# Optimization experiments

Hardware: AMD Instinct MI355X
Metric: run time of the kernel (lower is better)

## Reference

```python
import jax, jax.numpy as jnp
import numpy as np

NUM_EXPERTS = 8
TOP_K = 2


def setup_inputs() -> dict:
    key = jax.random.key(0)
    ks = jax.random.split(key, 6)
    B, S, D, F, E = 2, 2048, 512, 1536, NUM_EXPERTS
    scale = 0.02
    return {
        "x": jax.random.normal(ks[0], (B, S, D), dtype=jnp.float32),
        "Wg": jax.random.normal(ks[1], (D, E), dtype=jnp.float32) * scale,
        "W1": jax.random.normal(ks[2], (E, D, F), dtype=jnp.float32) * scale,
        "W2": jax.random.normal(ks[3], (E, F, D), dtype=jnp.float32) * scale,
        "W3": jax.random.normal(ks[4], (E, D, F), dtype=jnp.float32) * scale,
        "b3": jax.random.normal(ks[5], (E, F), dtype=jnp.float32) * scale,
    }


def reference(x, Wg, W1, W2, W3, b3):
    # Router (eval mode: no noise). x: [B,S,D]
    logits = jnp.einsum("bsd,de->bse", x, Wg)  # [B,S,E]
    top_logits, top_idx = jax.lax.top_k(logits, TOP_K)  # [B,S,K]
    top_w = jax.nn.softmax(top_logits, axis=-1)  # [B,S,K]
    # Combine weights per expert: scatter top-k weights into E slots.
    onehot = jax.nn.one_hot(top_idx, NUM_EXPERTS, dtype=x.dtype)  # [B,S,K,E]
    C = jnp.sum(onehot * top_w[..., None], axis=-2)  # [B,S,E]
    # Dense per-expert SwiGLU FFN; non-selected experts contribute weight 0,
    # so the math matches the original masked gather/scatter exactly.
    h = jnp.einsum("bsd,edf->bsef", x, W1)  # [B,S,E,F]
    g = jnp.einsum("bsd,edf->bsef", x, W3) + b3  # [B,S,E,F]
    act = jax.nn.silu(h) * g  # [B,S,E,F]
    out = jnp.einsum("bse,bsef,efd->bsd", C, act, W2)  # [B,S,D]
    return out
```

## Files before the change

### kernel.cpp

```cpp
#include <hip/hip_runtime.h>

constexpr int NTOK = 4096;
constexpr int DIM  = 512;
constexpr int FF   = 1536;
constexpr int NE   = 8;
constexpr int CAP  = 4096;

typedef __attribute__((ext_vector_type(8))) short short8;
typedef __attribute__((ext_vector_type(4))) float f32x4;

static __device__ __forceinline__ unsigned short f2bf(float f) {
    unsigned int x = __float_as_uint(f);
    unsigned int r = x + 0x7fffu + ((x >> 16) & 1u);
    return (unsigned short)(r >> 16);
}

static __device__ __forceinline__ void gload_lds16(const void* g, void* l) {
    __builtin_amdgcn_global_load_lds(
        (const __attribute__((address_space(1))) unsigned int*)g,
        (__attribute__((address_space(3))) unsigned int*)l, 16, 0, 0);
}

__global__ __launch_bounds__(256) void moe_router(
    const float* __restrict__ x, const float* __restrict__ wg,
    int* __restrict__ eidx, float* __restrict__ wts)
{
    int lane = threadIdx.x & 63;
    int wave = threadIdx.x >> 6;
    int tok  = blockIdx.x * 4 + wave;

    float acc[NE];
#pragma unroll
    for (int e = 0; e < NE; ++e) acc[e] = 0.f;

    const float* xr = x + (size_t)tok * DIM;
#pragma unroll
    for (int i = 0; i < DIM / 64; ++i) {
        int d = i * 64 + lane;
        float xv = xr[d];
        const float4* wr = (const float4*)(wg + (size_t)d * NE);
        float4 w0 = wr[0], w1 = wr[1];
        acc[0] += xv * w0.x; acc[1] += xv * w0.y; acc[2] += xv * w0.z; acc[3] += xv * w0.w;
        acc[4] += xv * w1.x; acc[5] += xv * w1.y; acc[6] += xv * w1.z; acc[7] += xv * w1.w;
    }
#pragma unroll
    for (int e = 0; e < NE; ++e) {
#pragma unroll
        for (int off = 32; off >= 1; off >>= 1)
            acc[e] += __shfl_xor(acc[e], off, 64);
    }
    if (lane == 0) {
        int i0 = 0; float m0 = acc[0];
#pragma unroll
        for (int e = 1; e < NE; ++e) if (acc[e] > m0) { m0 = acc[e]; i0 = e; }
        int i1 = -1; float m1 = -3.4e38f;
#pragma unroll
        for (int e = 0; e < NE; ++e) if (e != i0 && acc[e] > m1) { m1 = acc[e]; i1 = e; }
        float e1 = expf(m1 - m0);
        float s  = 1.f + e1;
        int s0 = tok * 2, s1 = tok * 2 + 1;
        wts[s0] = 1.f / s;
        wts[s1] = e1 / s;
        eidx[s0] = i0;
        eidx[s1] = i1;
    }
}

__global__ __launch_bounds__(256) void moe_build_lists(
    const int* __restrict__ eidx, int* __restrict__ cnt, int* __restrict__ lists)
{
    int e = blockIdx.x;
    __shared__ int s_base;
    __shared__ int s_wcnt[4];
    if (threadIdx.x == 0) s_base = 0;
    __syncthreads();
    int lane = threadIdx.x & 63, wv = threadIdx.x >> 6;
    for (int c = 0; c < 2 * NTOK; c += 256) {
        int slot = c + threadIdx.x;
        bool m = (eidx[slot] == e);
        unsigned long long bal = __ballot(m);
        if (lane == 0) s_wcnt[wv] = __popcll(bal);
        __syncthreads();
        int wbase = s_base;
        for (int i = 0; i < wv; ++i) wbase += s_wcnt[i];
        if (m) {
            int off = __popcll(bal & ((1ull << lane) - 1ull));
            lists[e * CAP + wbase + off] = slot;
        }
        __syncthreads();
        if (threadIdx.x == 0) s_base += s_wcnt[0] + s_wcnt[1] + s_wcnt[2] + s_wcnt[3];
        __syncthreads();
    }
    if (threadIdx.x == 0) cnt[e] = s_base;
}

__global__ __launch_bounds__(256) void cvt_x(
    const float* __restrict__ x, unsigned short* __restrict__ xbf)
{
    int i = (blockIdx.x * 256 + threadIdx.x) * 8;
    float4 a = *(const float4*)(x + i);
    float4 b = *(const float4*)(x + i + 4);
    ushort4 o0, o1;
    o0.x = f2bf(a.x); o0.y = f2bf(a.y); o0.z = f2bf(a.z); o0.w = f2bf(a.w);
    o1.x = f2bf(b.x); o1.y = f2bf(b.y); o1.z = f2bf(b.z); o1.w = f2bf(b.w);
    *(ushort4*)(xbf + i)     = o0;
    *(ushort4*)(xbf + i + 4) = o1;
}

__global__ __launch_bounds__(256) void transpose_cvt(
    const float* __restrict__ in, unsigned short* __restrict__ out, int R, int C)
{
    __shared__ float tile[64][65];
    int c0 = blockIdx.x * 64;
    int r0 = blockIdx.y * 64;
    int z  = blockIdx.z;
    const float* ip = in + (size_t)z * R * C;
    char* op = (char*)(out + (size_t)z * R * C);

    int tr = threadIdx.x >> 4;
    int tc = (threadIdx.x & 15) * 4;
#pragma unroll
    for (int p = 0; p < 4; ++p) {
        int r = p * 16 + tr;
        float4 v = *(const float4*)(ip + (size_t)(r0 + r) * C + c0 + tc);
        tile[r][tc + 0] = v.x; tile[r][tc + 1] = v.y;
        tile[r][tc + 2] = v.z; tile[r][tc + 3] = v.w;
    }
    __syncthreads();
#pragma unroll
    for (int p = 0; p < 4; ++p) {
        int c = p * 16 + tr;
        ushort4 o;
        o.x = f2bf(tile[tc + 0][c]);
        o.y = f2bf(tile[tc + 1][c]);
        o.z = f2bf(tile[tc + 2][c]);
        o.w = f2bf(tile[tc + 3][c]);
        int cb = ((r0 + tc) * 2) ^ ((c & 7) << 4);
        *(ushort4*)(op + (size_t)(c0 + c) * (R * 2) + cb) = o;
    }
}

__global__ __launch_bounds__(256) void moe_ffn1(
    const unsigned short* __restrict__ xbf,
    const unsigned short* __restrict__ w1t,
    const unsigned short* __restrict__ w3t,
    const float* __restrict__ b3,
    const int* __restrict__ cnt, const int* __restrict__ lists,
    unsigned short* __restrict__ act)
{
    int e    = blockIdx.y >> 5;
    int mb   = blockIdx.y & 31;
    int n0   = blockIdx.x * 64;
    int ce   = cnt[e];
    int row0 = mb * 128;
    if (row0 >= ce) return;

    __shared__ int s_slot[128];
    __shared__ __attribute__((aligned(16))) char sA [128 * 128];
    __shared__ __attribute__((aligned(16))) char sB1[64 * 128];
    __shared__ __attribute__((aligned(16))) char sB3[64 * 128];

    int tid = threadIdx.x;
    if (tid < 128) {
        int r = row0 + tid;
        s_slot[tid] = (r < ce) ? lists[e * CAP + r] : lists[e * CAP + row0];
    }
    __syncthreads();

    int lane = tid & 63;
    int wv   = tid >> 6;
    int wm   = wv >> 1, wn = wv & 1;

    int lrow = lane >> 3;
    int lcol = (lane & 7) * 16;
    int aswz = lcol ^ (lrow << 4);
    const char* aSrc[4];
#pragma unroll
    for (int i = 0; i < 4; ++i) {
        int rr  = i * 32 + wv * 8 + lrow;
        int tok = s_slot[rr] >> 1;
        aSrc[i] = (const char*)xbf + (size_t)tok * (DIM * 2) + aswz;
    }
    const char* b1Src[2]; const char* b3Src[2];
#pragma unroll
    for (int i = 0; i < 2; ++i) {
        int rr = i * 32 + wv * 8 + lrow;
        size_t rb = ((size_t)e * FF + n0 + rr) * (DIM * 2) + lcol;
        b1Src[i] = (const char*)w1t + rb;
        b3Src[i] = (const char*)w3t + rb;
    }

    f32x4 acch[4][2], accg[4][2];
#pragma unroll
    for (int i = 0; i < 4; ++i)
#pragma unroll
        for (int j = 0; j < 2; ++j) { acch[i][j] = (f32x4)0.f; accg[i][j] = (f32x4)0.f; }

    for (int kc = 0; kc < DIM * 2; kc += 128) {
#pragma unroll
        for (int i = 0; i < 4; ++i)
            gload_lds16(aSrc[i] + kc, sA + (i * 32 + wv * 8) * 128);
#pragma unroll
        for (int i = 0; i < 2; ++i) {
            gload_lds16(b1Src[i] + kc, sB1 + (i * 32 + wv * 8) * 128);
            gload_lds16(b3Src[i] + kc, sB3 + (i * 32 + wv * 8) * 128);
        }
        __syncthreads();

#pragma unroll
        for (int ks = 0; ks < 2; ++ks) {
            short8 af[4], b1f[2], b3f[2];
#pragma unroll
            for (int mi = 0; mi < 4; ++mi) {
                int row = wm * 64 + mi * 16 + (lane & 15);
                int ba  = row * 128 + ((ks * 64 + (lane >> 4) * 16) ^ ((row & 7) << 4));
                af[mi] = *(const short8*)(sA + ba);
            }
#pragma unroll
            for (int ni = 0; ni < 2; ++ni) {
                int row = wn * 32 + ni * 16 + (lane & 15);
                int ba  = row * 128 + ((ks * 64 + (lane >> 4) * 16) ^ ((row & 7) << 4));
                b1f[ni] = *(const short8*)(sB1 + ba);
                b3f[ni] = *(const short8*)(sB3 + ba);
            }
#pragma unroll
            for (int mi = 0; mi < 4; ++mi)
#pragma unroll
                for (int ni = 0; ni < 2; ++ni) {
                    acch[mi][ni] = __builtin_amdgcn_mfma_f32_16x16x32_bf16(af[mi], b1f[ni], acch[mi][ni], 0, 0, 0);
                    accg[mi][ni] = __builtin_amdgcn_mfma_f32_16x16x32_bf16(af[mi], b3f[ni], accg[mi][ni], 0, 0, 0);
                }
        }
        __syncthreads();
    }

#pragma unroll
    for (int ni = 0; ni < 2; ++ni) {
        int fcol = n0 + wn * 32 + ni * 16 + (lane & 15);
        float b3v = b3[e * FF + fcol];
#pragma unroll
        for (int mi = 0; mi < 4; ++mi) {
            int rl = wm * 64 + mi * 16 + (lane >> 4) * 4;
#pragma unroll
            for (int r = 0; r < 4; ++r) {
                int rg = rl + r;
                if (row0 + rg < ce) {
                    float h = acch[mi][ni][r];
                    float g = accg[mi][ni][r] + b3v;
                    float a = (h / (1.f + __expf(-h))) * g;
                    act[(size_t)s_slot[rg] * FF + fcol] = f2bf(a);
                }
            }
        }
    }
}

__global__ __launch_bounds__(256) void moe_ffn2(
    const unsigned short* __restrict__ act,
    const unsigned short* __restrict__ w2t,
    const int* __restrict__ cnt, const int* __restrict__ lists,
    const float* __restrict__ wts,
    float* __restrict__ yws)
{
    int e    = blockIdx.y >> 5;
    int mb   = blockIdx.y & 31;
    int n0   = blockIdx.x * 64;
    int ce   = cnt[e];
    int row0 = mb * 128;
    if (row0 >= ce) return;

    __shared__ int   s_slot[128];
    __shared__ float s_w[128];
    __shared__ __attribute__((aligned(16))) char sA[128 * 128];
    __shared__ __attribute__((aligned(16))) char sB[64 * 128];

    int tid = threadIdx.x;
    if (tid < 128) {
        int r  = row0 + tid;
        int sl = (r < ce) ? lists[e * CAP + r] : lists[e * CAP + row0];
        s_slot[tid] = sl;
        s_w[tid]    = wts[sl];
    }
    __syncthreads();

    int lane = tid & 63;
    int wv   = tid >> 6;
    int wm   = wv >> 1, wn = wv & 1;

    int lrow = lane >> 3;
    int lcol = (lane & 7) * 16;
    int aswz = lcol ^ (lrow << 4);
    const char* aSrc[4];
#pragma unroll
    for (int i = 0; i < 4; ++i) {
        int rr = i * 32 + wv * 8 + lrow;
        aSrc[i] = (const char*)act + (size_t)s_slot[rr] * (FF * 2) + aswz;
    }
    const char* bSrc[2];
#pragma unroll
    for (int i = 0; i < 2; ++i) {
        int rr = i * 32 + wv * 8 + lrow;
        bSrc[i] = (const char*)w2t + ((size_t)e * DIM + n0 + rr) * (FF * 2) + lcol;
    }

    f32x4 acc[4][2];
#pragma unroll
    for (int i = 0; i < 4; ++i)
#pragma unroll
        for (int j = 0; j < 2; ++j) acc[i][j] = (f32x4)0.f;

    for (int kc = 0; kc < FF * 2; kc += 128) {
#pragma unroll
        for (int i = 0; i < 4; ++i)
            gload_lds16(aSrc[i] + kc, sA + (i * 32 + wv * 8) * 128);
#pragma unroll
        for (int i = 0; i < 2; ++i)
            gload_lds16(bSrc[i] + kc, sB + (i * 32 + wv * 8) * 128);
        __syncthreads();

#pragma unroll
        for (int ks = 0; ks < 2; ++ks) {
            short8 af[4], bf[2];
#pragma unroll
            for (int mi = 0; mi < 4; ++mi) {
                int row = wm * 64 + mi * 16 + (lane & 15);
                int ba  = row * 128 + ((ks * 64 + (lane >> 4) * 16) ^ ((row & 7) << 4));
                af[mi] = *(const short8*)(sA + ba);
            }
#pragma unroll
            for (int ni = 0; ni < 2; ++ni) {
                int row = wn * 32 + ni * 16 + (lane & 15);
                int ba  = row * 128 + ((ks * 64 + (lane >> 4) * 16) ^ ((row & 7) << 4));
                bf[ni] = *(const short8*)(sB + ba);
            }
#pragma unroll
            for (int mi = 0; mi < 4; ++mi)
#pragma unroll
                for (int ni = 0; ni < 2; ++ni)
                    acc[mi][ni] = __builtin_amdgcn_mfma_f32_16x16x32_bf16(af[mi], bf[ni], acc[mi][ni], 0, 0, 0);
        }
        __syncthreads();
    }

#pragma unroll
    for (int mi = 0; mi < 4; ++mi) {
#pragma unroll
        for (int r = 0; r < 4; ++r) {
            int rg = wm * 64 + mi * 16 + (lane >> 4) * 4 + r;
            if (row0 + rg < ce) {
                float w  = s_w[rg];
                int slot = s_slot[rg];
#pragma unroll
                for (int ni = 0; ni < 2; ++ni) {
                    int dd = n0 + wn * 32 + ni * 16 + (lane & 15);
                    yws[(size_t)slot * DIM + dd] = acc[mi][ni][r] * w;
                }
            }
        }
    }
}

__global__ __launch_bounds__(256) void moe_combine(
    const float* __restrict__ yws, float* __restrict__ out)
{
    int i  = blockIdx.x * 256 + threadIdx.x;
    int t  = i >> 7;
    int d4 = (i & 127) * 4;
    const float4* y0 = (const float4*)(yws + ((size_t)(2 * t)     * DIM + d4));
    const float4* y1 = (const float4*)(yws + ((size_t)(2 * t + 1) * DIM + d4));
    float4 a = *y0, b = *y1;
    float4 o = make_float4(a.x + b.x, a.y + b.y, a.z + b.z, a.w + b.w);
    *(float4*)(out + (size_t)t * DIM + d4) = o;
}

extern "C" void kernel_launch(void* const* d_in, const int* in_sizes, int n_in,
                              void* d_out, int out_size, void* d_ws, size_t ws_size,
                              hipStream_t stream)
{
    const float* x  = (const float*)d_in[0];
    const float* wg = (const float*)d_in[1];
    const float* w1 = (const float*)d_in[2];
    const float* w2 = (const float*)d_in[3];
    const float* w3 = (const float*)d_in[4];
    const float* b3 = (const float*)d_in[5];
    float* out = (float*)d_out;
    char*  ws  = (char*)d_ws;

    int*   cnt   = (int*)ws;
    int*   lists = (int*)(ws + 256);
    float* wts   = (float*)(ws + 256 + NE * CAP * 4);
    int*   eidx  = (int*)(ws + 256 + NE * CAP * 4 + NTOK * 2 * 4);
    size_t off   = 256 + (size_t)NE * CAP * 4 + (size_t)NTOK * 2 * 4 * 2;

    constexpr size_t WSZ = (size_t)NE * DIM * FF;
    unsigned short* w2t = (unsigned short*)(ws + off);
    unsigned short* w1t = w2t + WSZ;
    unsigned short* w3t = w1t + WSZ;
    unsigned short* act = w3t + WSZ;
    unsigned short* xbf = w2t;
    float*          yws = (float*)w1t;

    moe_router<<<NTOK / 4, 256, 0, stream>>>(x, wg, eidx, wts);
    moe_build_lists<<<NE, 256, 0, stream>>>(eidx, cnt, lists);
    cvt_x<<<NTOK * DIM / 8 / 256, 256, 0, stream>>>(x, xbf);

    dim3 tgA(FF / 64, DIM / 64, NE);
    transpose_cvt<<<tgA, 256, 0, stream>>>(w1, w1t, DIM, FF);
    transpose_cvt<<<tgA, 256, 0, stream>>>(w3, w3t, DIM, FF);

    dim3 g1(FF / 64, NE * 32);
    moe_ffn1<<<g1, 256, 0, stream>>>(xbf, w1t, w3t, b3, cnt, lists, act);

    dim3 tgB(DIM / 64, FF / 64, NE);
    transpose_cvt<<<tgB, 256, 0, stream>>>(w2, w2t, FF, DIM);

    dim3 g2(DIM / 64, NE * 32);
    moe_ffn2<<<g2, 256, 0, stream>>>(act, w2t, cnt, lists, wts, yws);

    moe_combine<<<(NTOK * DIM / 4) / 256, 256, 0, stream>>>(yws, out);
}
```

Baseline: 266.0 us.

## Parallelize routing lists, fuse conversions, compact activations, widen FFN1 tiles

Several changes land together. The bf16 conversion of x moves into the router kernel, and the serial per-expert list build is replaced by a parallel count-then-scatter into one compact list. The W1/W3 transposes are merged into a single launch. FFN1 now uses 128-wide N tiles and writes activations contiguously per expert through an LDS-staged, swizzled coalesced store, so FFN2 reads contiguous rows instead of gathering by slot. FFN2 also stages its output through LDS for float4 scattered stores. The cost is larger register and LDS use in FFN1, which may lower occupancy.

```diff
diff --git a/kernel.cpp b/kernel.cpp
--- a/kernel.cpp
+++ b/kernel.cpp
@@ -4,7 +4,6 @@
 constexpr int DIM  = 512;
 constexpr int FF   = 1536;
 constexpr int NE   = 8;
-constexpr int CAP  = 4096;
 
 typedef __attribute__((ext_vector_type(8))) short short8;
 typedef __attribute__((ext_vector_type(4))) float f32x4;
@@ -23,7 +22,7 @@
 
 __global__ __launch_bounds__(256) void moe_router(
     const float* __restrict__ x, const float* __restrict__ wg,
-    int* __restrict__ eidx, float* __restrict__ wts)
+    int* __restrict__ eidx, float* __restrict__ wts, unsigned short* __restrict__ xbf)
 {
     int lane = threadIdx.x & 63;
     int wave = threadIdx.x >> 6;
@@ -34,10 +33,12 @@
     for (int e = 0; e < NE; ++e) acc[e] = 0.f;
 
     const float* xr = x + (size_t)tok * DIM;
+    unsigned short* xo = xbf + (size_t)tok * DIM;
 #pragma unroll
     for (int i = 0; i < DIM / 64; ++i) {
         int d = i * 64 + lane;
         float xv = xr[d];
+        xo[d] = f2bf(xv);
         const float4* wr = (const float4*)(wg + (size_t)d * NE);
         float4 w0 = wr[0], w1 = wr[1];
         acc[0] += xv * w0.x; acc[1] += xv * w0.y; acc[2] += xv * w0.z; acc[3] += xv * w0.w;
@@ -66,56 +67,77 @@
     }
 }
 
-__global__ __launch_bounds__(256) void moe_build_lists(
-    const int* __restrict__ eidx, int* __restrict__ cnt, int* __restrict__ lists)
-{
-    int e = blockIdx.x;
-    __shared__ int s_base;
-    __shared__ int s_wcnt[4];
-    if (threadIdx.x == 0) s_base = 0;
-    __syncthreads();
-    int lane = threadIdx.x & 63, wv = threadIdx.x >> 6;
-    for (int c = 0; c < 2 * NTOK; c += 256) {
-        int slot = c + threadIdx.x;
-        bool m = (eidx[slot] == e);
-        unsigned long long bal = __ballot(m);
-        if (lane == 0) s_wcnt[wv] = __popcll(bal);
-        __syncthreads();
-        int wbase = s_base;
-        for (int i = 0; i < wv; ++i) wbase += s_wcnt[i];
-        if (m) {
-            int off = __popcll(bal & ((1ull << lane) - 1ull));
-            lists[e * CAP + wbase + off] = slot;
-        }
-        __syncthreads();
-        if (threadIdx.x == 0) s_base += s_wcnt[0] + s_wcnt[1] + s_wcnt[2] + s_wcnt[3];
-        __syncthreads();
-    }
-    if (threadIdx.x == 0) cnt[e] = s_base;
-}
-
-__global__ __launch_bounds__(256) void cvt_x(
-    const float* __restrict__ x, unsigned short* __restrict__ xbf)
-{
-    int i = (blockIdx.x * 256 + threadIdx.x) * 8;
-    float4 a = *(const float4*)(x + i);
-    float4 b = *(const float4*)(x + i + 4);
-    ushort4 o0, o1;
-    o0.x = f2bf(a.x); o0.y = f2bf(a.y); o0.z = f2bf(a.z); o0.w = f2bf(a.w);
-    o1.x = f2bf(b.x); o1.y = f2bf(b.y); o1.z = f2bf(b.z); o1.w = f2bf(b.w);
-    *(ushort4*)(xbf + i)     = o0;
-    *(ushort4*)(xbf + i + 4) = o1;
-}
-
-__global__ __launch_bounds__(256) void transpose_cvt(
-    const float* __restrict__ in, unsigned short* __restrict__ out, int R, int C)
+__global__ __launch_bounds__(256) void moe_count(
+    const int* __restrict__ eidx, int* __restrict__ pcnt)
+{
+    __shared__ int s_wc[4][8];
+    int tid = threadIdx.x, lane = tid & 63, wv = tid >> 6;
+    int e = eidx[blockIdx.x * 256 + tid];
+#pragma unroll
+    for (int e0 = 0; e0 < 8; ++e0) {
+        unsigned long long bal = __ballot(e == e0);
+        if (lane == 0) s_wc[wv][e0] = __popcll(bal);
+    }
+    __syncthreads();
+    if (tid < 8)
+        pcnt[blockIdx.x * 8 + tid] = s_wc[0][tid] + s_wc[1][tid] + s_wc[2][tid] + s_wc[3][tid];
+}
+
+__global__ __launch_bounds__(256) void moe_scatter(
+    const int* __restrict__ eidx, const int* __restrict__ pcnt,
+    int* __restrict__ clist, int* __restrict__ cnt, int* __restrict__ ebase)
+{
+    __shared__ int s_all[256];
+    __shared__ int s_wc[4][8];
+    int tid = threadIdx.x, bx = blockIdx.x;
+    int lane = tid & 63, wv = tid >> 6;
+    s_all[tid] = pcnt[tid];
+    int slot = bx * 256 + tid;
+    int e = eidx[slot];
+    int myoff = 0;
+#pragma unroll
+    for (int e0 = 0; e0 < 8; ++e0) {
+        unsigned long long bal = __ballot(e == e0);
+        if (lane == 0) s_wc[wv][e0] = __popcll(bal);
+        if (e == e0) myoff = __popcll(bal & ((1ull << lane) - 1ull));
+    }
+    __syncthreads();
+    int base = 0;
+#pragma unroll
+    for (int ep = 0; ep < 8; ++ep) {
+        int t = 0;
+        for (int b = 0; b < 32; ++b) t += s_all[b * 8 + ep];
+        if (ep < e) base += (t + 7) & ~7;
+    }
+    int cbase = 0;
+    for (int b = 0; b < bx; ++b) cbase += s_all[b * 8 + e];
+    int wbase = 0;
+    for (int w = 0; w < wv; ++w) wbase += s_wc[w][e];
+    clist[base + cbase + wbase + myoff] = slot;
+    if (bx == 0 && tid == 0) {
+        int eb = 0;
+        for (int ep = 0; ep < 8; ++ep) {
+            int t = 0;
+            for (int b = 0; b < 32; ++b) t += s_all[b * 8 + ep];
+            cnt[ep] = t;
+            ebase[ep] = eb;
+            eb += (t + 7) & ~7;
+        }
+    }
+}
+
+__global__ __launch_bounds__(256) void transpose_cvt2(
+    const float* __restrict__ inA, unsigned short* __restrict__ outA,
+    const float* __restrict__ inB, unsigned short* __restrict__ outB,
+    int R, int C)
 {
     __shared__ float tile[64][65];
-    int c0 = blockIdx.x * 64;
-    int r0 = blockIdx.y * 64;
-    int z  = blockIdx.z;
-    const float* ip = in + (size_t)z * R * C;
-    char* op = (char*)(out + (size_t)z * R * C);
+    int c0 = blockIdx.x * 64, r0 = blockIdx.y * 64, z = blockIdx.z;
+    const float* in      = (z < 8) ? inA  : inB;
+    unsigned short* out  = (z < 8) ? outA : outB;
+    int zz = z & 7;
+    const float* ip = in + (size_t)zz * R * C;
+    char* op = (char*)(out + (size_t)zz * R * C);
 
     int tr = threadIdx.x >> 4;
     int tc = (threadIdx.x & 15) * 4;
@@ -140,13 +162,133 @@
     }
 }
 
-__global__ __launch_bounds__(256) void moe_ffn1(
+__global__ __launch_bounds__(256, 2) void moe_ffn1(
     const unsigned short* __restrict__ xbf,
     const unsigned short* __restrict__ w1t,
     const unsigned short* __restrict__ w3t,
     const float* __restrict__ b3,
-    const int* __restrict__ cnt, const int* __restrict__ lists,
-    unsigned short* __restrict__ act)
+    const int* __restrict__ cnt, const int* __restrict__ ebase,
+    const int* __restrict__ clist,
+    unsigned short* __restrict__ actc)
+{
+    int e    = blockIdx.y >> 5;
+    int mb   = blockIdx.y & 31;
+    int n0   = blockIdx.x * 128;
+    int ce   = cnt[e];
+    int row0 = mb * 128;
+    if (row0 >= ce) return;
+    int eb   = ebase[e];
+
+    __shared__ __attribute__((aligned(16))) char smem[49152];
+    __shared__ int s_slot[128];
+    char* sA  = smem;
+    char* sB1 = smem + 16384;
+    char* sB3 = smem + 32768;
+
+    int tid = threadIdx.x;
+    if (tid < 128) {
+        int r = row0 + tid;
+        s_slot[tid] = (r < ce) ? clist[eb + r] : clist[eb + row0];
+    }
+    __syncthreads();
+
+    int lane = tid & 63, wv = tid >> 6;
+    int wm = wv >> 1, wn = wv & 1;
+    int lrow = lane >> 3;
+    int lcol = (lane & 7) * 16;
+    int aswz = lcol ^ (lrow << 4);
+
+    const char* aSrc[4]; const char* b1Src[4]; const char* b3Src[4];
+#pragma unroll
+    for (int i = 0; i < 4; ++i) {
+        int rr = i * 32 + wv * 8 + lrow;
+        aSrc[i] = (const char*)xbf + (size_t)(s_slot[rr] >> 1) * (DIM * 2) + aswz;
+        size_t rb = ((size_t)e * FF + n0 + rr) * (DIM * 2) + lcol;
+        b1Src[i] = (const char*)w1t + rb;
+        b3Src[i] = (const char*)w3t + rb;
+    }
+
+    f32x4 acch[4][4], accg[4][4];
+#pragma unroll
+    for (int i = 0; i < 4; ++i)
+#pragma unroll
+        for (int j = 0; j < 4; ++j) { acch[i][j] = (f32x4)0.f; accg[i][j] = (f32x4)0.f; }
+
+    for (int kc = 0; kc < DIM * 2; kc += 128) {
+#pragma unroll
+        for (int i = 0; i < 4; ++i) {
+            int ro = (i * 32 + wv * 8) * 128;
+            gload_lds16(aSrc[i]  + kc, sA  + ro);
+            gload_lds16(b1Src[i] + kc, sB1 + ro);
+            gload_lds16(b3Src[i] + kc, sB3 + ro);
+        }
+        __syncthreads();
+
+#pragma unroll
+        for (int ks = 0; ks < 2; ++ks) {
+            short8 af[4], b1f[4], b3f[4];
+#pragma unroll
+            for (int mi = 0; mi < 4; ++mi) {
+                int row = wm * 64 + mi * 16 + (lane & 15);
+                int ba  = row * 128 + ((ks * 64 + (lane >> 4) * 16) ^ ((row & 7) << 4));
+                af[mi] = *(const short8*)(sA + ba);
+            }
+#pragma unroll
+            for (int ni = 0; ni < 4; ++ni) {
+                int row = wn * 64 + ni * 16 + (lane & 15);
+                int ba  = row * 128 + ((ks * 64 + (lane >> 4) * 16) ^ ((row & 7) << 4));
+                b1f[ni] = *(const short8*)(sB1 + ba);
+                b3f[ni] = *(const short8*)(sB3 + ba);
+            }
+#pragma unroll
+            for (int mi = 0; mi < 4; ++mi)
+#pragma unroll
+                for (int ni = 0; ni < 4; ++ni) {
+                    acch[mi][ni] = __builtin_amdgcn_mfma_f32_16x16x32_bf16(af[mi], b1f[ni], acch[mi][ni], 0, 0, 0);
+                    accg[mi][ni] = __builtin_amdgcn_mfma_f32_16x16x32_bf16(af[mi], b3f[ni], accg[mi][ni], 0, 0, 0);
+                }
+        }
+        __syncthreads();
+    }
+
+    char* sE = smem;
+#pragma unroll
+    for (int ni = 0; ni < 4; ++ni) {
+        int col = wn * 64 + ni * 16 + (lane & 15);
+        float b3v = b3[e * FF + n0 + col];
+#pragma unroll
+        for (int mi = 0; mi < 4; ++mi) {
+            int rbase = wm * 64 + mi * 16 + (lane >> 4) * 4;
+#pragma unroll
+            for (int r = 0; r < 4; ++r) {
+                float h = acch[mi][ni][r];
+                float g = accg[mi][ni][r] + b3v;
+                float a = (h / (1.f + __expf(-h))) * g;
+                *(unsigned short*)(sE + (rbase + r) * 256 + col * 2) = f2bf(a);
+            }
+        }
+    }
+    __syncthreads();
+
+    int lim = ce - row0;
+#pragma unroll
+    for (int it = 0; it < 8; ++it) {
+        int chunk = it * 256 + tid;
+        int row = chunk >> 4, c8 = chunk & 15;
+        if (row < lim) {
+            int crow = eb + row0 + row;
+            size_t dst = (size_t)crow * (FF * 2) + n0 * 2 + ((c8 * 16) ^ ((crow & 7) << 4));
+            *(short8*)((char*)actc + dst) = *(const short8*)(sE + row * 256 + c8 * 16);
+        }
+    }
+}
+
+__global__ __launch_bounds__(256) void moe_ffn2(
+    const unsigned short* __restrict__ actc,
+    const unsigned short* __restrict__ w2t,
+    const int* __restrict__ cnt, const int* __restrict__ ebase,
+    const int* __restrict__ clist, const float* __restrict__ wts,
+    float* __restrict__ yws)
 {
     int e    = blockIdx.y >> 5;
     int mb   = blockIdx.y & 31;
@@ -154,62 +296,60 @@
     int ce   = cnt[e];
     int row0 = mb * 128;
     if (row0 >= ce) return;
-
-    __shared__ int s_slot[128];
-    __shared__ __attribute__((aligned(16))) char sA [128 * 128];
-    __shared__ __attribute__((aligned(16))) char sB1[64 * 128];
-    __shared__ __attribute__((aligned(16))) char sB3[64 * 128];
+    int eb   = ebase[e];
+
+    __shared__ __attribute__((aligned(16))) char smem[32768];
+    __shared__ int   s_slot[128];
+    __shared__ float s_w[128];
+    char* sA = smem;
+    char* sB = smem + 16384;
 
     int tid = threadIdx.x;
     if (tid < 128) {
-        int r = row0 + tid;
-        s_slot[tid] = (r < ce) ? lists[e * CAP + r] : lists[e * CAP + row0];
-    }
-    __syncthreads();
-
-    int lane = tid & 63;
-    int wv   = tid >> 6;
-    int wm   = wv >> 1, wn = wv & 1;
-
+        int r  = row0 + tid;
+        int sl = (r < ce) ? clist[eb + r] : clist[eb + row0];
+        s_slot[tid] = sl;
+        s_w[tid]    = wts[sl];
+    }
+    __syncthreads();
+
+    int lane = tid & 63, wv = tid >> 6;
+    int wm = wv >> 1, wn = wv & 1;
     int lrow = lane >> 3;
     int lcol = (lane & 7) * 16;
-    int aswz = lcol ^ (lrow << 4);
+
     const char* aSrc[4];
 #pragma unroll
     for (int i = 0; i < 4; ++i) {
-        int rr  = i * 32 + wv * 8 + lrow;
-        int tok = s_slot[rr] >> 1;
-        aSrc[i] = (const char*)xbf + (size_t)tok * (DIM * 2) + aswz;
-    }
-    const char* b1Src[2]; const char* b3Src[2];
+        int rr = i * 32 + wv * 8 + lrow;
+        int cr = (row0 + rr < ce) ? (eb + row0 + rr) : (eb + row0);
+        aSrc[i] = (const char*)actc + (size_t)cr * (FF * 2) + lcol;
+    }
+    const char* bSrc[2];
 #pragma unroll
     for (int i = 0; i < 2; ++i) {
         int rr = i * 32 + wv * 8 + lrow;
-        size_t rb = ((size_t)e * FF + n0 + rr) * (DIM * 2) + lcol;
-        b1Src[i] = (const char*)w1t + rb;
-        b3Src[i] = (const char*)w3t + rb;
-    }
-
-    f32x4 acch[4][2], accg[4][2];
+        bSrc[i] = (const char*)w2t + ((size_t)e * DIM + n0 + rr) * (FF * 2) + lcol;
+    }
+
+    f32x4 acc[4][2];
 #pragma unroll
     for (int i = 0; i < 4; ++i)
 #pragma unroll
-        for (int j = 0; j < 2; ++j) { acch[i][j] = (f32x4)0.f; accg[i][j] = (f32x4)0.f; }
-
-    for (int kc = 0; kc < DIM * 2; kc += 128) {
+        for (int j = 0; j < 2; ++j) acc[i][j] = (f32x4)0.f;
+
+    for (int kc = 0; kc < FF * 2; kc += 128) {
 #pragma unroll
         for (int i = 0; i < 4; ++i)
             gload_lds16(aSrc[i] + kc, sA + (i * 32 + wv * 8) * 128);
 #pragma unroll
-        for (int i = 0; i < 2; ++i) {
-            gload_lds16(b1Src[i] + kc, sB1 + (i * 32 + wv * 8) * 128);
-            gload_lds16(b3Src[i] + kc, sB3 + (i * 32 + wv * 8) * 128);
-        }
+        for (int i = 0; i < 2; ++i)
+            gload_lds16(bSrc[i] + kc, sB + (i * 32 + wv * 8) * 128);
         __syncthreads();
 
 #pragma unroll
         for (int ks = 0; ks < 2; ++ks) {
-            short8 af[4], b1f[2], b3f[2];
+            short8 af[4], bf[2];
 #pragma unroll
             for (int mi = 0; mi < 4; ++mi) {
                 int row = wm * 64 + mi * 16 + (lane & 15);
@@ -220,117 +360,6 @@
             for (int ni = 0; ni < 2; ++ni) {
                 int row = wn * 32 + ni * 16 + (lane & 15);
                 int ba  = row * 128 + ((ks * 64 + (lane >> 4) * 16) ^ ((row & 7) << 4));
-                b1f[ni] = *(const short8*)(sB1 + ba);
-                b3f[ni] = *(const short8*)(sB3 + ba);
-            }
-#pragma unroll
-            for (int mi = 0; mi < 4; ++mi)
-#pragma unroll
-                for (int ni = 0; ni < 2; ++ni) {
-                    acch[mi][ni] = __builtin_amdgcn_mfma_f32_16x16x32_bf16(af[mi], b1f[ni], acch[mi][ni], 0, 0, 0);
-                    accg[mi][ni] = __builtin_amdgcn_mfma_f32_16x16x32_bf16(af[mi], b3f[ni], accg[mi][ni], 0, 0, 0);
-                }
-        }
-        __syncthreads();
-    }
-
-#pragma unroll
-    for (int ni = 0; ni < 2; ++ni) {
-        int fcol = n0 + wn * 32 + ni * 16 + (lane & 15);
-        float b3v = b3[e * FF + fcol];
-#pragma unroll
-        for (int mi = 0; mi < 4; ++mi) {
-            int rl = wm * 64 + mi * 16 + (lane >> 4) * 4;
-#pragma unroll
-            for (int r = 0; r < 4; ++r) {
-                int rg = rl + r;
-                if (row0 + rg < ce) {
-                    float h = acch[mi][ni][r];
-                    float g = accg[mi][ni][r] + b3v;
-                    float a = (h / (1.f + __expf(-h))) * g;
-                    act[(size_t)s_slot[rg] * FF + fcol] = f2bf(a);
-                }
-            }
-        }
-    }
-}
-
-__global__ __launch_bounds__(256) void moe_ffn2(
-    const unsigned short* __restrict__ act,
-    const unsigned short* __restrict__ w2t,
-    const int* __restrict__ cnt, const int* __restrict__ lists,
-    const float* __restrict__ wts,
-    float* __restrict__ yws)
-{
-    int e    = blockIdx.y >> 5;
-    int mb   = blockIdx.y & 31;
-    int n0   = blockIdx.x * 64;
-    int ce   = cnt[e];
-    int row0 = mb * 128;
-    if (row0 >= ce) return;
-
-    __shared__ int   s_slot[128];
-    __shared__ float s_w[128];
-    __shared__ __attribute__((aligned(16))) char sA[128 * 128];
-    __shared__ __attribute__((aligned(16))) char sB[64 * 128];
-
-    int tid = threadIdx.x;
-    if (tid < 128) {
-        int r  = row0 + tid;
-        int sl = (r < ce) ? lists[e * CAP + r] : lists[e * CAP + row0];
-        s_slot[tid] = sl;
-        s_w[tid]    = wts[sl];
-    }
-    __syncthreads();
-
-    int lane = tid & 63;
-    int wv   = tid >> 6;
-    int wm   = wv >> 1, wn = wv & 1;
-
-    int lrow = lane >> 3;
-    int lcol = (lane & 7) * 16;
-    int aswz = lcol ^ (lrow << 4);
-    const char* aSrc[4];
-#pragma unroll
-    for (int i = 0; i < 4; ++i) {
-        int rr = i * 32 + wv * 8 + lrow;
-        aSrc[i] = (const char*)act + (size_t)s_slot[rr] * (FF * 2) + aswz;
-    }
-    const char* bSrc[2];
-#pragma unroll
-    for (int i = 0; i < 2; ++i) {
-        int rr = i * 32 + wv * 8 + lrow;
-        bSrc[i] = (const char*)w2t + ((size_t)e * DIM + n0 + rr) * (FF * 2) + lcol;
-    }
-
-    f32x4 acc[4][2];
-#pragma unroll
-    for (int i = 0; i < 4; ++i)
-#pragma unroll
-        for (int j = 0; j < 2; ++j) acc[i][j] = (f32x4)0.f;
-
-    for (int kc = 0; kc < FF * 2; kc += 128) {
-#pragma unroll
-        for (int i = 0; i < 4; ++i)
-            gload_lds16(aSrc[i] + kc, sA + (i * 32 + wv * 8) * 128);
-#pragma unroll
-        for (int i = 0; i < 2; ++i)
-            gload_lds16(bSrc[i] + kc, sB + (i * 32 + wv * 8) * 128);
-        __syncthreads();
-
-#pragma unroll
-        for (int ks = 0; ks < 2; ++ks) {
-            short8 af[4], bf[2];
-#pragma unroll
-            for (int mi = 0; mi < 4; ++mi) {
-                int row = wm * 64 + mi * 16 + (lane & 15);
-                int ba  = row * 128 + ((ks * 64 + (lane >> 4) * 16) ^ ((row & 7) << 4));
-                af[mi] = *(const short8*)(sA + ba);
-            }
-#pragma unroll
-            for (int ni = 0; ni < 2; ++ni) {
-                int row = wn * 32 + ni * 16 + (lane & 15);
-                int ba  = row * 128 + ((ks * 64 + (lane >> 4) * 16) ^ ((row & 7) << 4));
                 bf[ni] = *(const short8*)(sB + ba);
             }
 #pragma unroll
@@ -342,21 +371,31 @@
         __syncthreads();
     }
 
+    char* sE = smem;
 #pragma unroll
     for (int mi = 0; mi < 4; ++mi) {
+        int rbase = wm * 64 + mi * 16 + (lane >> 4) * 4;
 #pragma unroll
         for (int r = 0; r < 4; ++r) {
-            int rg = wm * 64 + mi * 16 + (lane >> 4) * 4 + r;
-            if (row0 + rg < ce) {
-                float w  = s_w[rg];
-                int slot = s_slot[rg];
-#pragma unroll
-                for (int ni = 0; ni < 2; ++ni) {
-                    int dd = n0 + wn * 32 + ni * 16 + (lane & 15);
-                    yws[(size_t)slot * DIM + dd] = acc[mi][ni][r] * w;
-                }
-            }
-        }
+            int row = rbase + r;
+            float w = s_w[row];
+#pragma unroll
+            for (int ni = 0; ni < 2; ++ni) {
+                int col = wn * 32 + ni * 16 + (lane & 15);
+                *(float*)(sE + row * 256 + col * 4) = acc[mi][ni][r] * w;
+            }
+        }
+    }
+    __syncthreads();
+
+    int lim = ce - row0;
+#pragma unroll
+    for (int it = 0; it < 8; ++it) {
+        int chunk = it * 256 + tid;
+        int row = chunk >> 4, c4 = chunk & 15;
+        if (row < lim)
+            *(float4*)(yws + (size_t)s_slot[row] * DIM + n0 + c4 * 4) =
+                *(const float4*)(sE + row * 256 + c4 * 16);
     }
 }
 
@@ -386,36 +425,36 @@
     float* out = (float*)d_out;
     char*  ws  = (char*)d_ws;
 
-    int*   cnt   = (int*)ws;
-    int*   lists = (int*)(ws + 256);
-    float* wts   = (float*)(ws + 256 + NE * CAP * 4);
-    int*   eidx  = (int*)(ws + 256 + NE * CAP * 4 + NTOK * 2 * 4);
-    size_t off   = 256 + (size_t)NE * CAP * 4 + (size_t)NTOK * 2 * 4 * 2;
-
-    constexpr size_t WSZ = (size_t)NE * DIM * FF;
-    unsigned short* w2t = (unsigned short*)(ws + off);
-    unsigned short* w1t = w2t + WSZ;
-    unsigned short* w3t = w1t + WSZ;
-    unsigned short* act = w3t + WSZ;
-    unsigned short* xbf = w2t;
-    float*          yws = (float*)w1t;
-
-    moe_router<<<NTOK / 4, 256, 0, stream>>>(x, wg, eidx, wts);
-    moe_build_lists<<<NE, 256, 0, stream>>>(eidx, cnt, lists);
-    cvt_x<<<NTOK * DIM / 8 / 256, 256, 0, stream>>>(x, xbf);
-
-    dim3 tgA(FF / 64, DIM / 64, NE);
-    transpose_cvt<<<tgA, 256, 0, stream>>>(w1, w1t, DIM, FF);
-    transpose_cvt<<<tgA, 256, 0, stream>>>(w3, w3t, DIM, FF);
-
-    dim3 g1(FF / 64, NE * 32);
-    moe_ffn1<<<g1, 256, 0, stream>>>(xbf, w1t, w3t, b3, cnt, lists, act);
-
-    dim3 tgB(DIM / 64, FF / 64, NE);
-    transpose_cvt<<<tgB, 256, 0, stream>>>(w2, w2t, FF, DIM);
+    int*   cnt   = (int*)(ws + 0);
+    int*   ebase = (int*)(ws + 64);
+    int*   pcnt  = (int*)(ws + 256);
+    int*   eidx  = (int*)(ws + 2048);
+    float* wts   = (float*)(ws + 2048 + 32768);
+    int*   clist = (int*)(ws + 2048 + 65536);
+    constexpr size_t OFF_BIG = 102400;
+    constexpr size_t WB = (size_t)NE * DIM * FF * 2;
+    unsigned short* w2t  = (unsigned short*)(ws + OFF_BIG);
+    unsigned short* w1t  = (unsigned short*)(ws + OFF_BIG + WB);
+    unsigned short* w3t  = (unsigned short*)(ws + OFF_BIG + 2 * WB);
+    unsigned short* actc = (unsigned short*)(ws + OFF_BIG + 3 * WB);
+    unsigned short* xbf  = w2t;
+    float*          yws  = (float*)w1t;
+
+    moe_router <<<NTOK / 4, 256, 0, stream>>>(x, wg, eidx, wts, xbf);
+    moe_count  <<<32, 256, 0, stream>>>(eidx, pcnt);
+    moe_scatter<<<32, 256, 0, stream>>>(eidx, pcnt, clist, cnt, ebase);
+
+    dim3 tgA(FF / 64, DIM / 64, 16);
+    transpose_cvt2<<<tgA, 256, 0, stream>>>(w1, w1t, w3, w3t, DIM, FF);
+
+    dim3 g1(FF / 128, NE * 32);
+    moe_ffn1<<<g1, 256, 0, stream>>>(xbf, w1t, w3t, b3, cnt, ebase, clist, actc);
+
+    dim3 tgB(DIM / 64, FF / 64, 8);
+    transpose_cvt2<<<tgB, 256, 0, stream>>>(w2, w2t, w2, w2t, FF, DIM);
 
     dim3 g2(DIM / 64, NE * 32);
-    moe_ffn2<<<g2, 256, 0, stream>>>(act, w2t, cnt, lists, wts, yws);
+    moe_ffn2<<<g2, 256, 0, stream>>>(actc, w2t, cnt, ebase, clist, wts, yws);
 
     moe_combine<<<(NTOK * DIM / 4) / 256, 256, 0, stream>>>(yws, out);
 }
```

Measured after the change: 222.8 us. 1.19x faster.
